# Optimization experiments

Measured on AMD Instinct MI355X. Metric: run time of the kernel, lower is better.

## Reference

```python
import jax, jax.numpy as jnp
import numpy as np
from jax import lax

B, S, H = 64, 512, 768
L = 20          # num_labels
MAX_SPANS = 8   # span_number_classifier has MAX_SPANS+1 outputs


def setup_inputs() -> dict:
    key = jax.random.key(0)
    k = jax.random.split(key, 8)
    w = lambda i, shape: jax.random.normal(k[i], shape, jnp.float32) * 0.02
    return {
        "tokens_rep": jax.random.normal(k[0], (B, S, H), jnp.float32),
        "seq_rep": jax.random.normal(k[1], (B, H), jnp.float32),
        "w_start": w(2, (H,)), "b_start": jnp.zeros((), jnp.float32),
        "w_end": w(3, (H,)), "b_end": jnp.zeros((), jnp.float32),
        "W_nspans": w(4, (H, MAX_SPANS + 1)), "b_nspans": jnp.zeros((MAX_SPANS + 1,), jnp.float32),
        "W_span": w(5, (H, L)), "b_span": jnp.zeros((L,), jnp.float32),
        "W_pol": w(6, (H + L, L)), "b_pol": jnp.zeros((L,), jnp.float32),
    }


def _select_spans(ss, es, n_spans):
    """Faithful port of get_top_spans_nongreedy's while-loop.
    ss/es: [MAX_SPANS] ascending-sorted top indices (sentinel S beyond n_spans).
    Each iteration advances s_idx and/or e_idx, so 2*MAX_SPANS steps suffice."""
    def body(i, st):
        s_idx, e_idx, last_end, rem, out_s, out_e, cnt = st
        active = (rem > 0) & (s_idx < n_spans) & (e_idx < n_spans)
        s = ss[jnp.minimum(s_idx, MAX_SPANS - 1)]
        e = es[jnp.minimum(e_idx, MAX_SPANS - 1)]
        accept = active & (e > s) & (s >= last_end)
        inc_e = active & (~accept) & (e <= s)
        inc_s = active & (~accept) & (e > s)
        out_s = jnp.where(accept, out_s.at[cnt].set(s), out_s)
        out_e = jnp.where(accept, out_e.at[cnt].set(e), out_e)
        last_end = jnp.where(accept, e, last_end)
        a = accept.astype(jnp.int32)
        return (s_idx + a + inc_s.astype(jnp.int32),
                e_idx + a + inc_e.astype(jnp.int32),
                last_end, rem - a, out_s, out_e, cnt + a)

    z = jnp.zeros((MAX_SPANS,), jnp.int32)
    init = (jnp.int32(0), jnp.int32(0), jnp.int32(0), n_spans, z, z, jnp.int32(0))
    st = lax.fori_loop(0, 2 * MAX_SPANS, body, init)
    return st[4], st[5], st[6]  # starts, ends, count


def _per_item(tokens, starts, ends, fsl, n_spans, W_span, b_span):
    # sigmoid is monotone, so top-k of sigmoid(logits) == top-k of logits
    _, i_s = lax.top_k(starts, MAX_SPANS)
    _, i_e = lax.top_k(ends, MAX_SPANS)
    rank = jnp.arange(MAX_SPANS)
    keep = rank < n_spans
    ss = jnp.sort(jnp.where(keep, i_s, S).astype(jnp.int32))  # sentinel S sorts last
    es = jnp.sort(jnp.where(keep, i_e, S).astype(jnp.int32))
    out_s, out_e, cnt = _select_spans(ss, es, n_spans)
    valid = rank < cnt
    vf = valid.astype(tokens.dtype)

    # span mean-pooling tokens[s:e+1].mean(0) via a [MAX_SPANS,S] mask matmul
    t = jnp.arange(S)
    span_mask = ((t[None, :] >= out_s[:, None]) & (t[None, :] <= out_e[:, None])).astype(tokens.dtype)
    lengths = (out_e - out_s + 1).astype(tokens.dtype)
    span_vecs = (span_mask @ tokens) / lengths[:, None]         # [MAX_SPANS, H]

    mls = jax.nn.softmax(span_vecs @ W_span + b_span, axis=1)   # [MAX_SPANS, L]
    span_labels = jnp.argmax(mls, axis=1)
    fsl_soft = jax.nn.softmax(fsl)
    has_valid = cnt > 0

    labels_oh_m = jnp.zeros((L,), tokens.dtype).at[span_labels].max(vf)
    labels_oh_m = jnp.where(has_valid, labels_oh_m,
                            jnp.zeros((L,), tokens.dtype).at[jnp.argmax(fsl_soft)].set(1.0))
    spans_m = jnp.max(jnp.where(valid[:, None], mls, -jnp.inf), axis=0)
    spans_m = jnp.where(has_valid, spans_m, jnp.zeros((L,), tokens.dtype))
    starts_oh_m = jnp.zeros((S,), tokens.dtype).at[out_s].max(vf)
    ends_oh_m = jnp.zeros((S,), tokens.dtype).at[out_e].max(vf)

    # n_spans <= 1 branch
    labels_oh_1 = jnp.zeros((L,), tokens.dtype).at[jnp.argmax(fsl_soft)].set(1.0)
    starts_oh_1 = jnp.zeros((S,), tokens.dtype).at[jnp.argmax(starts)].set(1.0)
    ends_oh_1 = jnp.zeros((S,), tokens.dtype).at[jnp.argmax(ends)].set(1.0)

    single = n_spans <= 1
    spans = jnp.where(single, fsl_soft, spans_m)
    labels_oh = jnp.where(single, labels_oh_1, labels_oh_m)
    starts_oh = jnp.where(single, starts_oh_1, starts_oh_m)
    ends_oh = jnp.where(single, ends_oh_1, ends_oh_m)
    return spans, starts_oh, ends_oh, labels_oh


def reference(tokens_rep, seq_rep, w_start, b_start, w_end, b_end,
              W_nspans, b_nspans, W_span, b_span, W_pol, b_pol):
    full_seq_logits = seq_rep @ W_span + b_span        # [B, L]
    start_logits = tokens_rep @ w_start + b_start      # [B, S]
    end_logits = tokens_rep @ w_end + b_end            # [B, S]
    n_spans_logits = seq_rep @ W_nspans + b_nspans     # [B, MAX_SPANS+1]
    all_n_spans = jnp.argmax(n_spans_logits, axis=1).astype(jnp.int32)

    spans, starts_oh, ends_oh, labels_oh = jax.vmap(
        _per_item, in_axes=(0, 0, 0, 0, 0, None, None)
    )(tokens_rep, start_logits, end_logits, full_seq_logits, all_n_spans, W_span, b_span)

    pol_logits = jnp.concatenate([seq_rep, spans], axis=1) @ W_pol + b_pol
    return (start_logits, end_logits, spans, n_spans_logits, pol_logits,
            starts_oh, ends_oh, labels_oh)
```

## Files before the change

kernel.cpp:

```cpp
#include <hip/hip_runtime.h>
#include <math.h>

#define NB 64
#define SS 512
#define HH 768
#define LL 20
#define MS 8
#define NSPC 9

#define OFF_START 0
#define OFF_END   (NB*SS)
#define OFF_SPANS (2*NB*SS)
#define OFF_NSP   (2*NB*SS + NB*LL)
#define OFF_POL   (2*NB*SS + NB*LL + NB*NSPC)
#define OFF_SOH   (2*NB*SS + 2*NB*LL + NB*NSPC)
#define OFF_EOH   (3*NB*SS + 2*NB*LL + NB*NSPC)
#define OFF_LOH   (4*NB*SS + 2*NB*LL + NB*NSPC)

struct WS {
  float fsl[NB][LL];
  float mls[NB][MS][LL];
  int   nspans[NB];
  int   fslarg[NB];
  int   cnt[NB];
  int   out_s[NB][MS];
  int   out_e[NB][MS];
  int   slabel[NB][MS];
};

__global__ __launch_bounds__(256) void k0_seq(
    const float* __restrict__ seq,
    const float* __restrict__ Wspan, const float* __restrict__ bspan,
    const float* __restrict__ Wnsp,  const float* __restrict__ bnsp,
    float* __restrict__ out, WS* __restrict__ ws)
{
  int b = blockIdx.x;
  __shared__ float sh[HH];
  __shared__ float logits[LL + NSPC];
  int t = threadIdx.x;
  for (int i = t; i < HH; i += 256) sh[i] = seq[b*HH + i];
  __syncthreads();
  int wave = t >> 6, lane = t & 63;
  for (int o = wave; o < LL + NSPC; o += 4) {
    float acc = 0.f;
    if (o < LL) {
      for (int k = 0; k < HH/64; ++k) { int h = lane + 64*k; acc += sh[h] * Wspan[h*LL + o]; }
    } else {
      int j = o - LL;
      for (int k = 0; k < HH/64; ++k) { int h = lane + 64*k; acc += sh[h] * Wnsp[h*NSPC + j]; }
    }
    for (int off = 32; off >= 1; off >>= 1) acc += __shfl_down(acc, off);
    if (lane == 0) logits[o] = acc + (o < LL ? bspan[o] : bnsp[o - LL]);
  }
  __syncthreads();
  if (t == 0) {
    int bi = 0; float bv = logits[LL];
    for (int j = 1; j < NSPC; ++j) { float v = logits[LL + j]; if (v > bv) { bv = v; bi = j; } }
    ws->nspans[b] = bi;
    int fi = 0; float fv = logits[0];
    for (int j = 1; j < LL; ++j) { float v = logits[j]; if (v > fv) { fv = v; fi = j; } }
    ws->fslarg[b] = fi;
  }
  if (t < LL)  ws->fsl[b][t] = logits[t];
  if (t < NSPC) out[OFF_NSP + b*NSPC + t] = logits[LL + t];
}

__global__ __launch_bounds__(256) void k1_logits(
    const float4* __restrict__ tok,
    const float* __restrict__ wstart, const float* __restrict__ bstart,
    const float* __restrict__ wend,  const float* __restrict__ bend,
    float* __restrict__ out)
{
  __shared__ float4 shs[HH/4], she[HH/4];
  int t = threadIdx.x;
  const float4* wsg = (const float4*)wstart;
  const float4* weg = (const float4*)wend;
  for (int i = t; i < HH/4; i += 256) { shs[i] = wsg[i]; she[i] = weg[i]; }
  __syncthreads();
  int wave = t >> 6, lane = t & 63;
  int r = blockIdx.x * 4 + wave;
  const float4* row = tok + (size_t)r * (HH/4);
  float as = 0.f, ae = 0.f;
  for (int k = 0; k < 3; ++k) {
    int idx = k*64 + lane;
    float4 x = row[idx];
    float4 a = shs[idx]; float4 c = she[idx];
    as += x.x*a.x + x.y*a.y + x.z*a.z + x.w*a.w;
    ae += x.x*c.x + x.y*c.y + x.z*c.z + x.w*c.w;
  }
  for (int off = 32; off >= 1; off >>= 1) { as += __shfl_down(as, off); ae += __shfl_down(ae, off); }
  if (lane == 0) {
    out[OFF_START + r] = as + bstart[0];
    out[OFF_END   + r] = ae + bend[0];
  }
}

__global__ __launch_bounds__(256) void k2_select(
    float* __restrict__ out, WS* __restrict__ ws)
{
  int b = blockIdx.x;
  int t = threadIdx.x;
  int wave = t >> 6, lane = t & 63;

  __shared__ float candV[2][32];
  __shared__ int   candI[2][32];
  __shared__ int   topI[2][MS];
  __shared__ int   sh_cnt, sh_single;
  __shared__ int   sh_os[MS], sh_oe[MS];

  float sv0 = out[OFF_START + b*SS + t];
  float sv1 = out[OFF_START + b*SS + t + 256];
  float ev0 = out[OFF_END   + b*SS + t];
  float ev1 = out[OFF_END   + b*SS + t + 256];
  int   si0 = t, si1 = t + 256, ei0 = t, ei1 = t + 256;

  #pragma unroll
  for (int k = 0; k < MS; ++k) {
    float lvS = sv0; int liS = si0;
    if (sv1 > lvS) { lvS = sv1; liS = si1; }
    float lvE = ev0; int liE = ei0;
    if (ev1 > lvE) { lvE = ev1; liE = ei1; }
    #pragma unroll
    for (int m = 32; m >= 1; m >>= 1) {
      float ovS = __shfl_xor(lvS, m); int oiS = __shfl_xor(liS, m);
      if (ovS > lvS || (ovS == lvS && oiS < liS)) { lvS = ovS; liS = oiS; }
      float ovE = __shfl_xor(lvE, m); int oiE = __shfl_xor(liE, m);
      if (ovE > lvE || (ovE == lvE && oiE < liE)) { lvE = ovE; liE = oiE; }
    }
    if (lane == 0) {
      candV[0][wave*MS + k] = lvS; candI[0][wave*MS + k] = liS;
      candV[1][wave*MS + k] = lvE; candI[1][wave*MS + k] = liE;
    }
    if (si0 == liS) sv0 = -INFINITY;
    if (si1 == liS) sv1 = -INFINITY;
    if (ei0 == liE) ev0 = -INFINITY;
    if (ei1 == liE) ev1 = -INFINITY;
  }
  __syncthreads();

  if (wave < 2) {
    float v = -INFINITY; int idx = 0x7fffffff;
    if (lane < 32) { v = candV[wave][lane]; idx = candI[wave][lane]; }
    int rank = 0;
    #pragma unroll
    for (int j = 0; j < 32; ++j) {
      float vj = __shfl(v, j); int ij = __shfl(idx, j);
      if (vj > v || (vj == v && ij < idx)) ++rank;
    }
    if (lane < 32 && rank < MS) topI[wave][rank] = idx;
  }
  __syncthreads();

  if (wave == 0) {
    int n = ws->nspans[b];
    int xs = SS, xe = SS;
    if (lane < MS && lane < n) { xs = topI[0][lane]; xe = topI[1][lane]; }
    int rs = 0, re = 0;
    #pragma unroll
    for (int j = 0; j < MS; ++j) {
      int xj = __shfl(xs, j);
      if (xj < xs || (xj == xs && j < lane)) ++rs;
      int yj = __shfl(xe, j);
      if (yj < xe || (yj == xe && j < lane)) ++re;
    }
    int ss_srt = 0, es_srt = 0;
    #pragma unroll
    for (int j = 0; j < MS; ++j) {
      int xj = __shfl(xs, j); int rj = __shfl(rs, j);
      if (rj == lane) ss_srt = xj;
      int yj = __shfl(xe, j); int qj = __shfl(re, j);
      if (qj == lane) es_srt = yj;
    }
    int si = 0, ei = 0, last = 0, rem = n, cnt = 0;
    int my_os = 0, my_oe = 0;
    for (int it = 0; it < 2*MS; ++it) {
      bool active = (rem > 0) && (si < n) && (ei < n);
      int s = __shfl(ss_srt, si < MS ? si : MS - 1);
      int e = __shfl(es_srt, ei < MS ? ei : MS - 1);
      bool accept = active && (e > s) && (s >= last);
      bool ince = active && !accept && (e <= s);
      bool incs = active && !accept && (e > s);
      if (accept) {
        if (lane == cnt) { my_os = s; my_oe = e; }
        last = e; ++cnt; --rem; ++si; ++ei;
      } else {
        si += incs ? 1 : 0; ei += ince ? 1 : 0;
      }
    }
    if (lane < MS) {
      sh_os[lane] = my_os; sh_oe[lane] = my_oe;
      ws->out_s[b][lane] = my_os; ws->out_e[b][lane] = my_oe;
    }
    if (lane == 0) {
      sh_cnt = cnt; sh_single = (n <= 1) ? 1 : 0;
      ws->cnt[b] = cnt;
    }
  }
  __syncthreads();

  int cnt = sh_cnt, single = sh_single;
  for (int pos = t; pos < SS; pos += 256) {
    float sval = 0.f, eval = 0.f;
    if (single) {
      if (pos == topI[0][0]) sval = 1.f;
      if (pos == topI[1][0]) eval = 1.f;
    } else {
      for (int i = 0; i < cnt; ++i) {
        if (pos == sh_os[i]) sval = 1.f;
        if (pos == sh_oe[i]) eval = 1.f;
      }
    }
    out[OFF_SOH + b*SS + pos] = sval;
    out[OFF_EOH + b*SS + pos] = eval;
  }
}

__global__ __launch_bounds__(1024) void k3_pool(
    const float4* __restrict__ tok,
    const float* __restrict__ Wspan, const float* __restrict__ bspan,
    WS* __restrict__ ws)
{
  int b = blockIdx.x >> 3;
  int i = blockIdx.x & (MS - 1);
  if (i >= ws->cnt[b]) return;
  int s0 = ws->out_s[b][i], e0 = ws->out_e[b][i];
  int t = threadIdx.x;
  int g = t >> 8;
  int tid = t & 255;

  __shared__ float4 part[4][HH/4];
  __shared__ float pooled[HH];
  __shared__ float lg[LL];

  if (tid < HH/4) {
    float4 acc = make_float4(0.f, 0.f, 0.f, 0.f);
    const float4* base = tok + (size_t)b * SS * (HH/4) + tid;
    #pragma unroll 4
    for (int r = s0 + g; r <= e0; r += 4) {
      float4 x = base[(size_t)r * (HH/4)];
      acc.x += x.x; acc.y += x.y; acc.z += x.z; acc.w += x.w;
    }
    part[g][tid] = acc;
  }
  __syncthreads();

  if (t < HH/4) {
    float4 p0 = part[0][t], p1 = part[1][t], p2 = part[2][t], p3 = part[3][t];
    float inv = 1.f / (float)(e0 - s0 + 1);
    float4 s;
    s.x = (p0.x + p1.x + p2.x + p3.x) * inv;
    s.y = (p0.y + p1.y + p2.y + p3.y) * inv;
    s.z = (p0.z + p1.z + p2.z + p3.z) * inv;
    s.w = (p0.w + p1.w + p2.w + p3.w) * inv;
    ((float4*)pooled)[t] = s;
  }
  __syncthreads();

  int wave = t >> 6, lane = t & 63;
  for (int l = wave; l < LL; l += 16) {
    float acc = 0.f;
    for (int k = 0; k < HH/64; ++k) { int h = lane + 64*k; acc += pooled[h] * Wspan[h*LL + l]; }
    for (int off = 32; off >= 1; off >>= 1) acc += __shfl_down(acc, off);
    if (lane == 0) lg[l] = acc + bspan[l];
  }
  __syncthreads();

  if (t == 0) {
    float v[LL]; float mx = -INFINITY;
    #pragma unroll
    for (int l = 0; l < LL; ++l) { v[l] = lg[l]; mx = fmaxf(mx, v[l]); }
    int am = 0; float av = v[0];
    #pragma unroll
    for (int l = 1; l < LL; ++l) if (v[l] > av) { av = v[l]; am = l; }
    float sum = 0.f;
    #pragma unroll
    for (int l = 0; l < LL; ++l) { v[l] = expf(v[l] - mx); sum += v[l]; }
    float isum = 1.f / sum;
    #pragma unroll
    for (int l = 0; l < LL; ++l) ws->mls[b][i][l] = v[l] * isum;
    ws->slabel[b][i] = am;
  }
}

__global__ __launch_bounds__(256) void k4_final(
    const float* __restrict__ seq,
    const float* __restrict__ Wpol, const float* __restrict__ bpol,
    float* __restrict__ out, WS* __restrict__ ws)
{
  int b = blockIdx.x;
  int t = threadIdx.x;
  __shared__ float sp[LL];
  __shared__ float fsl_soft[LL];
  int n = ws->nspans[b];
  int single = (n <= 1) ? 1 : 0;
  int cnt = ws->cnt[b];
  int fa = ws->fslarg[b];
  if (t == 0) {
    float lg[LL]; float mx = -INFINITY;
    #pragma unroll
    for (int l = 0; l < LL; ++l) { lg[l] = ws->fsl[b][l]; mx = fmaxf(mx, lg[l]); }
    float sum = 0.f;
    #pragma unroll
    for (int l = 0; l < LL; ++l) { lg[l] = expf(lg[l] - mx); sum += lg[l]; }
    float isum = 1.f / sum;
    #pragma unroll
    for (int l = 0; l < LL; ++l) fsl_soft[l] = lg[l] * isum;
  }
  __syncthreads();
  if (t < LL) {
    float v;
    if (single) v = fsl_soft[t];
    else if (cnt > 0) { v = -INFINITY; for (int i = 0; i < cnt; ++i) v = fmaxf(v, ws->mls[b][i][t]); }
    else v = 0.f;
    sp[t] = v;
    out[OFF_SPANS + b*LL + t] = v;
    float lo = 0.f;
    if (single || cnt == 0) lo = (t == fa) ? 1.f : 0.f;
    else { for (int i = 0; i < cnt; ++i) if (ws->slabel[b][i] == t) lo = 1.f; }
    out[OFF_LOH + b*LL + t] = lo;
  }
  __syncthreads();
  int wave = t >> 6, lane = t & 63;
  const float* seqb = seq + b*HH;
  for (int l = wave; l < LL; l += 4) {
    float acc = 0.f;
    for (int k = 0; k < 13; ++k) {
      int h = lane + 64*k;
      if (h < HH + LL) {
        float v = (h < HH) ? seqb[h] : sp[h - HH];
        acc += v * Wpol[h*LL + l];
      }
    }
    for (int off = 32; off >= 1; off >>= 1) acc += __shfl_down(acc, off);
    if (lane == 0) out[OFF_POL + b*LL + l] = acc + bpol[l];
  }
}

extern "C" void kernel_launch(void* const* d_in, const int* in_sizes, int n_in,
                              void* d_out, int out_size, void* d_ws, size_t ws_size,
                              hipStream_t stream)
{
  const float* tok    = (const float*)d_in[0];
  const float* seq    = (const float*)d_in[1];
  const float* wstart = (const float*)d_in[2];
  const float* bstart = (const float*)d_in[3];
  const float* wend   = (const float*)d_in[4];
  const float* bend   = (const float*)d_in[5];
  const float* Wnsp   = (const float*)d_in[6];
  const float* bnsp   = (const float*)d_in[7];
  const float* Wspan  = (const float*)d_in[8];
  const float* bspan  = (const float*)d_in[9];
  const float* Wpol   = (const float*)d_in[10];
  const float* bpol   = (const float*)d_in[11];
  float* out = (float*)d_out;
  WS* ws = (WS*)d_ws;

  k0_seq  <<<NB, 256, 0, stream>>>(seq, Wspan, bspan, Wnsp, bnsp, out, ws);
  k1_logits<<<NB*SS/4, 256, 0, stream>>>((const float4*)tok, wstart, bstart, wend, bend, out);
  k2_select<<<NB, 256, 0, stream>>>(out, ws);
  k3_pool <<<NB*MS, 1024, 0, stream>>>((const float4*)tok, Wspan, bspan, ws);
  k4_final<<<NB, 256, 0, stream>>>(seq, Wpol, bpol, out, ws);
}
```

Before: 87.72 us.

## Fuse five kernels into two and process four token rows per wave

Merges the seq-logit kernel with the start/end logit kernel into one launch, with the blocks split by index, and has each wave compute four token rows instead of one. It also fuses span selection, span pooling, label softmax and the polarity head into a single 1024-thread block per batch item, keeping intermediates in shared memory instead of workspace. This removes three kernel launches and the global round-trips between them. The cost is that span pooling now runs serially per span inside only 64 blocks rather than across 512 blocks, which lowers parallelism on the pooling reads.

```diff
diff --git a/kernel.cpp b/kernel.cpp
--- a/kernel.cpp
+++ b/kernel.cpp
@@ -19,83 +19,90 @@
 
 struct WS {
   float fsl[NB][LL];
-  float mls[NB][MS][LL];
   int   nspans[NB];
   int   fslarg[NB];
-  int   cnt[NB];
-  int   out_s[NB][MS];
-  int   out_e[NB][MS];
-  int   slabel[NB][MS];
 };
 
-__global__ __launch_bounds__(256) void k0_seq(
+__global__ __launch_bounds__(256) void kA(
+    const float4* __restrict__ tok,
+    const float* __restrict__ wstart, const float* __restrict__ bstart,
+    const float* __restrict__ wend,  const float* __restrict__ bend,
     const float* __restrict__ seq,
     const float* __restrict__ Wspan, const float* __restrict__ bspan,
     const float* __restrict__ Wnsp,  const float* __restrict__ bnsp,
     float* __restrict__ out, WS* __restrict__ ws)
 {
-  int b = blockIdx.x;
-  __shared__ float sh[HH];
-  __shared__ float logits[LL + NSPC];
   int t = threadIdx.x;
-  for (int i = t; i < HH; i += 256) sh[i] = seq[b*HH + i];
-  __syncthreads();
   int wave = t >> 6, lane = t & 63;
-  for (int o = wave; o < LL + NSPC; o += 4) {
-    float acc = 0.f;
-    if (o < LL) {
-      for (int k = 0; k < HH/64; ++k) { int h = lane + 64*k; acc += sh[h] * Wspan[h*LL + o]; }
-    } else {
-      int j = o - LL;
-      for (int k = 0; k < HH/64; ++k) { int h = lane + 64*k; acc += sh[h] * Wnsp[h*NSPC + j]; }
-    }
-    for (int off = 32; off >= 1; off >>= 1) acc += __shfl_down(acc, off);
-    if (lane == 0) logits[o] = acc + (o < LL ? bspan[o] : bnsp[o - LL]);
-  }
-  __syncthreads();
-  if (t == 0) {
-    int bi = 0; float bv = logits[LL];
-    for (int j = 1; j < NSPC; ++j) { float v = logits[LL + j]; if (v > bv) { bv = v; bi = j; } }
-    ws->nspans[b] = bi;
-    int fi = 0; float fv = logits[0];
-    for (int j = 1; j < LL; ++j) { float v = logits[j]; if (v > fv) { fv = v; fi = j; } }
-    ws->fslarg[b] = fi;
-  }
-  if (t < LL)  ws->fsl[b][t] = logits[t];
-  if (t < NSPC) out[OFF_NSP + b*NSPC + t] = logits[LL + t];
+
+  if (blockIdx.x < 2048) {
+    __shared__ float4 shs[HH/4], she[HH/4];
+    const float4* wsg = (const float4*)wstart;
+    const float4* weg = (const float4*)wend;
+    for (int i = t; i < HH/4; i += 256) { shs[i] = wsg[i]; she[i] = weg[i]; }
+    __syncthreads();
+    int r0 = blockIdx.x * 16 + wave * 4;
+    const float4* base = tok + (size_t)r0 * (HH/4);
+    float as[4] = {0.f,0.f,0.f,0.f}, ae[4] = {0.f,0.f,0.f,0.f};
+    #pragma unroll
+    for (int k = 0; k < 3; ++k) {
+      int idx = k*64 + lane;
+      float4 a = shs[idx], c = she[idx];
+      #pragma unroll
+      for (int j = 0; j < 4; ++j) {
+        float4 x = base[(size_t)j * (HH/4) + idx];
+        as[j] += x.x*a.x + x.y*a.y + x.z*a.z + x.w*a.w;
+        ae[j] += x.x*c.x + x.y*c.y + x.z*c.z + x.w*c.w;
+      }
+    }
+    float b0 = bstart[0], b1 = bend[0];
+    #pragma unroll
+    for (int j = 0; j < 4; ++j) {
+      float a = as[j], e = ae[j];
+      for (int off = 32; off >= 1; off >>= 1) { a += __shfl_down(a, off); e += __shfl_down(e, off); }
+      if (lane == 0) {
+        out[OFF_START + r0 + j] = a + b0;
+        out[OFF_END   + r0 + j] = e + b1;
+      }
+    }
+  } else {
+    int b = blockIdx.x - 2048;
+    __shared__ float sh[HH];
+    __shared__ float logits[LL + NSPC];
+    for (int i = t; i < HH; i += 256) sh[i] = seq[b*HH + i];
+    __syncthreads();
+    for (int o = wave; o < LL + NSPC; o += 4) {
+      float acc = 0.f;
+      if (o < LL) {
+        for (int k = 0; k < HH/64; ++k) { int h = lane + 64*k; acc += sh[h] * Wspan[h*LL + o]; }
+      } else {
+        int j = o - LL;
+        for (int k = 0; k < HH/64; ++k) { int h = lane + 64*k; acc += sh[h] * Wnsp[h*NSPC + j]; }
+      }
+      for (int off = 32; off >= 1; off >>= 1) acc += __shfl_down(acc, off);
+      if (lane == 0) logits[o] = acc + (o < LL ? bspan[o] : bnsp[o - LL]);
+    }
+    __syncthreads();
+    if (t == 0) {
+      int bi = 0; float bv = logits[LL];
+      #pragma unroll
+      for (int j = 1; j < NSPC; ++j) { float v = logits[LL + j]; if (v > bv) { bv = v; bi = j; } }
+      ws->nspans[b] = bi;
+      int fi = 0; float fv = logits[0];
+      #pragma unroll
+      for (int j = 1; j < LL; ++j) { float v = logits[j]; if (v > fv) { fv = v; fi = j; } }
+      ws->fslarg[b] = fi;
+    }
+    if (t < LL)  ws->fsl[b][t] = logits[t];
+    if (t < NSPC) out[OFF_NSP + b*NSPC + t] = logits[LL + t];
+  }
 }
 
-__global__ __launch_bounds__(256) void k1_logits(
+__global__ __launch_bounds__(1024) void kBC(
     const float4* __restrict__ tok,
-    const float* __restrict__ wstart, const float* __restrict__ bstart,
-    const float* __restrict__ wend,  const float* __restrict__ bend,
-    float* __restrict__ out)
-{
-  __shared__ float4 shs[HH/4], she[HH/4];
-  int t = threadIdx.x;
-  const float4* wsg = (const float4*)wstart;
-  const float4* weg = (const float4*)wend;
-  for (int i = t; i < HH/4; i += 256) { shs[i] = wsg[i]; she[i] = weg[i]; }
-  __syncthreads();
-  int wave = t >> 6, lane = t & 63;
-  int r = blockIdx.x * 4 + wave;
-  const float4* row = tok + (size_t)r * (HH/4);
-  float as = 0.f, ae = 0.f;
-  for (int k = 0; k < 3; ++k) {
-    int idx = k*64 + lane;
-    float4 x = row[idx];
-    float4 a = shs[idx]; float4 c = she[idx];
-    as += x.x*a.x + x.y*a.y + x.z*a.z + x.w*a.w;
-    ae += x.x*c.x + x.y*c.y + x.z*c.z + x.w*c.w;
-  }
-  for (int off = 32; off >= 1; off >>= 1) { as += __shfl_down(as, off); ae += __shfl_down(ae, off); }
-  if (lane == 0) {
-    out[OFF_START + r] = as + bstart[0];
-    out[OFF_END   + r] = ae + bend[0];
-  }
-}
-
-__global__ __launch_bounds__(256) void k2_select(
+    const float* __restrict__ Wspan, const float* __restrict__ bspan,
+    const float* __restrict__ seq,
+    const float* __restrict__ Wpol, const float* __restrict__ bpol,
     float* __restrict__ out, WS* __restrict__ ws)
 {
   int b = blockIdx.x;
@@ -107,52 +114,61 @@
   __shared__ int   topI[2][MS];
   __shared__ int   sh_cnt, sh_single;
   __shared__ int   sh_os[MS], sh_oe[MS];
-
-  float sv0 = out[OFF_START + b*SS + t];
-  float sv1 = out[OFF_START + b*SS + t + 256];
-  float ev0 = out[OFF_END   + b*SS + t];
-  float ev1 = out[OFF_END   + b*SS + t + 256];
-  int   si0 = t, si1 = t + 256, ei0 = t, ei1 = t + 256;
-
-  #pragma unroll
-  for (int k = 0; k < MS; ++k) {
-    float lvS = sv0; int liS = si0;
-    if (sv1 > lvS) { lvS = sv1; liS = si1; }
-    float lvE = ev0; int liE = ei0;
-    if (ev1 > lvE) { lvE = ev1; liE = ei1; }
-    #pragma unroll
-    for (int m = 32; m >= 1; m >>= 1) {
-      float ovS = __shfl_xor(lvS, m); int oiS = __shfl_xor(liS, m);
-      if (ovS > lvS || (ovS == lvS && oiS < liS)) { lvS = ovS; liS = oiS; }
-      float ovE = __shfl_xor(lvE, m); int oiE = __shfl_xor(liE, m);
-      if (ovE > lvE || (ovE == lvE && oiE < liE)) { lvE = ovE; liE = oiE; }
-    }
-    if (lane == 0) {
-      candV[0][wave*MS + k] = lvS; candI[0][wave*MS + k] = liS;
-      candV[1][wave*MS + k] = lvE; candI[1][wave*MS + k] = liE;
-    }
-    if (si0 == liS) sv0 = -INFINITY;
-    if (si1 == liS) sv1 = -INFINITY;
-    if (ei0 == liE) ev0 = -INFINITY;
-    if (ei1 == liE) ev1 = -INFINITY;
-  }
-  __syncthreads();
-
-  if (wave < 2) {
+  __shared__ float4 part[5][HH/4];
+  __shared__ float pooled[HH];
+  __shared__ float slg[LL];
+  __shared__ float mls_s[MS][LL];
+  __shared__ int   slab_s[MS];
+  __shared__ float sp[LL], fsl_soft[LL];
+
+  int n = ws->nspans[b];
+
+  if (t < 256) {
+    float sv0 = out[OFF_START + b*SS + t];
+    float sv1 = out[OFF_START + b*SS + t + 256];
+    float ev0 = out[OFF_END   + b*SS + t];
+    float ev1 = out[OFF_END   + b*SS + t + 256];
+    int   si0 = t, si1 = t + 256, ei0 = t, ei1 = t + 256;
+    #pragma unroll
+    for (int k = 0; k < MS; ++k) {
+      float lvS = sv0; int liS = si0;
+      if (sv1 > lvS) { lvS = sv1; liS = si1; }
+      float lvE = ev0; int liE = ei0;
+      if (ev1 > lvE) { lvE = ev1; liE = ei1; }
+      #pragma unroll
+      for (int m = 32; m >= 1; m >>= 1) {
+        float ovS = __shfl_xor(lvS, m); int oiS = __shfl_xor(liS, m);
+        if (ovS > lvS || (ovS == lvS && oiS < liS)) { lvS = ovS; liS = oiS; }
+        float ovE = __shfl_xor(lvE, m); int oiE = __shfl_xor(liE, m);
+        if (ovE > lvE || (ovE == lvE && oiE < liE)) { lvE = ovE; liE = oiE; }
+      }
+      if (lane == 0) {
+        candV[0][wave*MS + k] = lvS; candI[0][wave*MS + k] = liS;
+        candV[1][wave*MS + k] = lvE; candI[1][wave*MS + k] = liE;
+      }
+      if (si0 == liS) sv0 = -INFINITY;
+      if (si1 == liS) sv1 = -INFINITY;
+      if (ei0 == liE) ev0 = -INFINITY;
+      if (ei1 == liE) ev1 = -INFINITY;
+    }
+  }
+  __syncthreads();
+
+  if (t < 128) {
+    int w = wave;
     float v = -INFINITY; int idx = 0x7fffffff;
-    if (lane < 32) { v = candV[wave][lane]; idx = candI[wave][lane]; }
+    if (lane < 32) { v = candV[w][lane]; idx = candI[w][lane]; }
     int rank = 0;
     #pragma unroll
     for (int j = 0; j < 32; ++j) {
       float vj = __shfl(v, j); int ij = __shfl(idx, j);
       if (vj > v || (vj == v && ij < idx)) ++rank;
     }
-    if (lane < 32 && rank < MS) topI[wave][rank] = idx;
+    if (lane < 32 && rank < MS) topI[w][rank] = idx;
   }
   __syncthreads();
 
   if (wave == 0) {
-    int n = ws->nspans[b];
     int xs = SS, xe = SS;
     if (lane < MS && lane < n) { xs = topI[0][lane]; xe = topI[1][lane]; }
     int rs = 0, re = 0;
@@ -187,19 +203,15 @@
         si += incs ? 1 : 0; ei += ince ? 1 : 0;
       }
     }
-    if (lane < MS) {
-      sh_os[lane] = my_os; sh_oe[lane] = my_oe;
-      ws->out_s[b][lane] = my_os; ws->out_e[b][lane] = my_oe;
-    }
-    if (lane == 0) {
-      sh_cnt = cnt; sh_single = (n <= 1) ? 1 : 0;
-      ws->cnt[b] = cnt;
-    }
+    if (lane < MS) { sh_os[lane] = my_os; sh_oe[lane] = my_oe; }
+    if (lane == 0) { sh_cnt = cnt; sh_single = (n <= 1) ? 1 : 0; }
   }
   __syncthreads();
 
   int cnt = sh_cnt, single = sh_single;
-  for (int pos = t; pos < SS; pos += 256) {
+
+  if (t < SS) {
+    int pos = t;
     float sval = 0.f, eval = 0.f;
     if (single) {
       if (pos == topI[0][0]) sval = 1.f;
@@ -213,87 +225,57 @@
     out[OFF_SOH + b*SS + pos] = sval;
     out[OFF_EOH + b*SS + pos] = eval;
   }
-}
-
-__global__ __launch_bounds__(1024) void k3_pool(
-    const float4* __restrict__ tok,
-    const float* __restrict__ Wspan, const float* __restrict__ bspan,
-    WS* __restrict__ ws)
-{
-  int b = blockIdx.x >> 3;
-  int i = blockIdx.x & (MS - 1);
-  if (i >= ws->cnt[b]) return;
-  int s0 = ws->out_s[b][i], e0 = ws->out_e[b][i];
-  int t = threadIdx.x;
-  int g = t >> 8;
-  int tid = t & 255;
-
-  __shared__ float4 part[4][HH/4];
-  __shared__ float pooled[HH];
-  __shared__ float lg[LL];
-
-  if (tid < HH/4) {
-    float4 acc = make_float4(0.f, 0.f, 0.f, 0.f);
-    const float4* base = tok + (size_t)b * SS * (HH/4) + tid;
-    #pragma unroll 4
-    for (int r = s0 + g; r <= e0; r += 4) {
-      float4 x = base[(size_t)r * (HH/4)];
-      acc.x += x.x; acc.y += x.y; acc.z += x.z; acc.w += x.w;
-    }
-    part[g][tid] = acc;
-  }
-  __syncthreads();
-
-  if (t < HH/4) {
-    float4 p0 = part[0][t], p1 = part[1][t], p2 = part[2][t], p3 = part[3][t];
-    float inv = 1.f / (float)(e0 - s0 + 1);
-    float4 s;
-    s.x = (p0.x + p1.x + p2.x + p3.x) * inv;
-    s.y = (p0.y + p1.y + p2.y + p3.y) * inv;
-    s.z = (p0.z + p1.z + p2.z + p3.z) * inv;
-    s.w = (p0.w + p1.w + p2.w + p3.w) * inv;
-    ((float4*)pooled)[t] = s;
-  }
-  __syncthreads();
-
-  int wave = t >> 6, lane = t & 63;
-  for (int l = wave; l < LL; l += 16) {
-    float acc = 0.f;
-    for (int k = 0; k < HH/64; ++k) { int h = lane + 64*k; acc += pooled[h] * Wspan[h*LL + l]; }
-    for (int off = 32; off >= 1; off >>= 1) acc += __shfl_down(acc, off);
-    if (lane == 0) lg[l] = acc + bspan[l];
-  }
-  __syncthreads();
-
-  if (t == 0) {
-    float v[LL]; float mx = -INFINITY;
-    #pragma unroll
-    for (int l = 0; l < LL; ++l) { v[l] = lg[l]; mx = fmaxf(mx, v[l]); }
-    int am = 0; float av = v[0];
-    #pragma unroll
-    for (int l = 1; l < LL; ++l) if (v[l] > av) { av = v[l]; am = l; }
-    float sum = 0.f;
-    #pragma unroll
-    for (int l = 0; l < LL; ++l) { v[l] = expf(v[l] - mx); sum += v[l]; }
-    float isum = 1.f / sum;
-    #pragma unroll
-    for (int l = 0; l < LL; ++l) ws->mls[b][i][l] = v[l] * isum;
-    ws->slabel[b][i] = am;
-  }
-}
-
-__global__ __launch_bounds__(256) void k4_final(
-    const float* __restrict__ seq,
-    const float* __restrict__ Wpol, const float* __restrict__ bpol,
-    float* __restrict__ out, WS* __restrict__ ws)
-{
-  int b = blockIdx.x;
-  int t = threadIdx.x;
-  __shared__ float sp[LL];
-  __shared__ float fsl_soft[LL];
-  int n = ws->nspans[b];
-  int single = (n <= 1) ? 1 : 0;
-  int cnt = ws->cnt[b];
+
+  int g = t / 192, q = t - g * 192;
+  for (int i = 0; i < cnt; ++i) {
+    int s0 = sh_os[i], e0 = sh_oe[i];
+    if (t < 960) {
+      float4 acc = make_float4(0.f, 0.f, 0.f, 0.f);
+      const float4* base = tok + (size_t)b * SS * (HH/4) + q;
+      #pragma unroll 4
+      for (int r = s0 + g; r <= e0; r += 5) {
+        float4 x = base[(size_t)r * (HH/4)];
+        acc.x += x.x; acc.y += x.y; acc.z += x.z; acc.w += x.w;
+      }
+      part[g][q] = acc;
+    }
+    __syncthreads();
+    if (t < HH/4) {
+      float inv = 1.f / (float)(e0 - s0 + 1);
+      float4 p0 = part[0][t], p1 = part[1][t], p2 = part[2][t], p3 = part[3][t], p4 = part[4][t];
+      float4 s;
+      s.x = (p0.x + p1.x + p2.x + p3.x + p4.x) * inv;
+      s.y = (p0.y + p1.y + p2.y + p3.y + p4.y) * inv;
+      s.z = (p0.z + p1.z + p2.z + p3.z + p4.z) * inv;
+      s.w = (p0.w + p1.w + p2.w + p3.w + p4.w) * inv;
+      ((float4*)pooled)[t] = s;
+    }
+    __syncthreads();
+    for (int l = wave; l < LL; l += 16) {
+      float acc = 0.f;
+      for (int k = 0; k < HH/64; ++k) { int h = lane + 64*k; acc += pooled[h] * Wspan[h*LL + l]; }
+      for (int off = 32; off >= 1; off >>= 1) acc += __shfl_down(acc, off);
+      if (lane == 0) slg[l] = acc + bspan[l];
+    }
+    __syncthreads();
+    if (t == 0) {
+      float v[LL]; float mx = -INFINITY;
+      #pragma unroll
+      for (int l = 0; l < LL; ++l) { v[l] = slg[l]; mx = fmaxf(mx, v[l]); }
+      int am = 0; float av = v[0];
+      #pragma unroll
+      for (int l = 1; l < LL; ++l) if (v[l] > av) { av = v[l]; am = l; }
+      float sum = 0.f;
+      #pragma unroll
+      for (int l = 0; l < LL; ++l) { v[l] = expf(v[l] - mx); sum += v[l]; }
+      float isum = 1.f / sum;
+      #pragma unroll
+      for (int l = 0; l < LL; ++l) mls_s[i][l] = v[l] * isum;
+      slab_s[i] = am;
+    }
+    __syncthreads();
+  }
+
   int fa = ws->fslarg[b];
   if (t == 0) {
     float lg[LL]; float mx = -INFINITY;
@@ -310,19 +292,18 @@
   if (t < LL) {
     float v;
     if (single) v = fsl_soft[t];
-    else if (cnt > 0) { v = -INFINITY; for (int i = 0; i < cnt; ++i) v = fmaxf(v, ws->mls[b][i][t]); }
+    else if (cnt > 0) { v = -INFINITY; for (int i = 0; i < cnt; ++i) v = fmaxf(v, mls_s[i][t]); }
     else v = 0.f;
     sp[t] = v;
     out[OFF_SPANS + b*LL + t] = v;
     float lo = 0.f;
     if (single || cnt == 0) lo = (t == fa) ? 1.f : 0.f;
-    else { for (int i = 0; i < cnt; ++i) if (ws->slabel[b][i] == t) lo = 1.f; }
+    else { for (int i = 0; i < cnt; ++i) if (slab_s[i] == t) lo = 1.f; }
     out[OFF_LOH + b*LL + t] = lo;
   }
   __syncthreads();
-  int wave = t >> 6, lane = t & 63;
   const float* seqb = seq + b*HH;
-  for (int l = wave; l < LL; l += 4) {
+  for (int l = wave; l < LL; l += 16) {
     float acc = 0.f;
     for (int k = 0; k < 13; ++k) {
       int h = lane + 64*k;
@@ -355,9 +336,8 @@
   float* out = (float*)d_out;
   WS* ws = (WS*)d_ws;
 
-  k0_seq  <<<NB, 256, 0, stream>>>(seq, Wspan, bspan, Wnsp, bnsp, out, ws);
-  k1_logits<<<NB*SS/4, 256, 0, stream>>>((const float4*)tok, wstart, bstart, wend, bend, out);
-  k2_select<<<NB, 256, 0, stream>>>(out, ws);
-  k3_pool <<<NB*MS, 1024, 0, stream>>>((const float4*)tok, Wspan, bspan, ws);
-  k4_final<<<NB, 256, 0, stream>>>(seq, Wpol, bpol, out, ws);
+  kA <<<2112, 256, 0, stream>>>((const float4*)tok, wstart, bstart, wend, bend,
+                                seq, Wspan, bspan, Wnsp, bnsp, out, ws);
+  kBC<<<NB, 1024, 0, stream>>>((const float4*)tok, Wspan, bspan,
+                               seq, Wpol, bpol, out, ws);
 }
```

Result: slower. 90.32 us (+3.0%).

## Merge seq-logit and token-logit kernels, process eight rows per wave

Applied to the files above, without the earlier changes.

Fuses the sequence-level classifier kernel and the start/end token-logit kernel into one launch. The first 1024 blocks compute start/end logits and the last 64 compute the sequence logits. Each wave now handles eight token rows instead of one, so the weight reads from shared memory are reused across rows, there are fewer blocks, and more loads are in flight. This removes one kernel launch and the weight-staging overhead per row. In exchange it uses more registers and runs fewer, longer blocks on the memory-bound pass over tokens.

```diff
diff --git a/kernel.cpp b/kernel.cpp
--- a/kernel.cpp
+++ b/kernel.cpp
@@ -28,74 +28,83 @@
   int   slabel[NB][MS];
 };
 
-__global__ __launch_bounds__(256) void k0_seq(
+__global__ __launch_bounds__(256) void kA(
+    const float4* __restrict__ tok,
+    const float* __restrict__ wstart, const float* __restrict__ bstart,
+    const float* __restrict__ wend,  const float* __restrict__ bend,
     const float* __restrict__ seq,
     const float* __restrict__ Wspan, const float* __restrict__ bspan,
     const float* __restrict__ Wnsp,  const float* __restrict__ bnsp,
     float* __restrict__ out, WS* __restrict__ ws)
 {
-  int b = blockIdx.x;
-  __shared__ float sh[HH];
-  __shared__ float logits[LL + NSPC];
   int t = threadIdx.x;
-  for (int i = t; i < HH; i += 256) sh[i] = seq[b*HH + i];
-  __syncthreads();
   int wave = t >> 6, lane = t & 63;
-  for (int o = wave; o < LL + NSPC; o += 4) {
-    float acc = 0.f;
-    if (o < LL) {
-      for (int k = 0; k < HH/64; ++k) { int h = lane + 64*k; acc += sh[h] * Wspan[h*LL + o]; }
-    } else {
-      int j = o - LL;
-      for (int k = 0; k < HH/64; ++k) { int h = lane + 64*k; acc += sh[h] * Wnsp[h*NSPC + j]; }
-    }
-    for (int off = 32; off >= 1; off >>= 1) acc += __shfl_down(acc, off);
-    if (lane == 0) logits[o] = acc + (o < LL ? bspan[o] : bnsp[o - LL]);
-  }
-  __syncthreads();
-  if (t == 0) {
-    int bi = 0; float bv = logits[LL];
-    for (int j = 1; j < NSPC; ++j) { float v = logits[LL + j]; if (v > bv) { bv = v; bi = j; } }
-    ws->nspans[b] = bi;
-    int fi = 0; float fv = logits[0];
-    for (int j = 1; j < LL; ++j) { float v = logits[j]; if (v > fv) { fv = v; fi = j; } }
-    ws->fslarg[b] = fi;
-  }
-  if (t < LL)  ws->fsl[b][t] = logits[t];
-  if (t < NSPC) out[OFF_NSP + b*NSPC + t] = logits[LL + t];
-}
-
-__global__ __launch_bounds__(256) void k1_logits(
-    const float4* __restrict__ tok,
-    const float* __restrict__ wstart, const float* __restrict__ bstart,
-    const float* __restrict__ wend,  const float* __restrict__ bend,
-    float* __restrict__ out)
-{
-  __shared__ float4 shs[HH/4], she[HH/4];
-  int t = threadIdx.x;
-  const float4* wsg = (const float4*)wstart;
-  const float4* weg = (const float4*)wend;
-  for (int i = t; i < HH/4; i += 256) { shs[i] = wsg[i]; she[i] = weg[i]; }
-  __syncthreads();
-  int wave = t >> 6, lane = t & 63;
-  int r = blockIdx.x * 4 + wave;
-  const float4* row = tok + (size_t)r * (HH/4);
-  float as = 0.f, ae = 0.f;
-  for (int k = 0; k < 3; ++k) {
-    int idx = k*64 + lane;
-    float4 x = row[idx];
-    float4 a = shs[idx]; float4 c = she[idx];
-    as += x.x*a.x + x.y*a.y + x.z*a.z + x.w*a.w;
-    ae += x.x*c.x + x.y*c.y + x.z*c.z + x.w*c.w;
-  }
-  for (int off = 32; off >= 1; off >>= 1) { as += __shfl_down(as, off); ae += __shfl_down(ae, off); }
-  if (lane == 0) {
-    out[OFF_START + r] = as + bstart[0];
-    out[OFF_END   + r] = ae + bend[0];
-  }
-}
-
-__global__ __launch_bounds__(256) void k2_select(
+
+  if (blockIdx.x < 1024) {
+    __shared__ float4 shs[HH/4], she[HH/4];
+    const float4* wsg = (const float4*)wstart;
+    const float4* weg = (const float4*)wend;
+    for (int i = t; i < HH/4; i += 256) { shs[i] = wsg[i]; she[i] = weg[i]; }
+    __syncthreads();
+    int r0 = blockIdx.x * 32 + wave * 8;
+    const float4* base = tok + (size_t)r0 * (HH/4);
+    float as[8] = {0.f,0.f,0.f,0.f,0.f,0.f,0.f,0.f};
+    float ae[8] = {0.f,0.f,0.f,0.f,0.f,0.f,0.f,0.f};
+    #pragma unroll
+    for (int k = 0; k < 3; ++k) {
+      int idx = k*64 + lane;
+      float4 a = shs[idx], c = she[idx];
+      #pragma unroll
+      for (int j = 0; j < 8; ++j) {
+        float4 x = base[(size_t)j * (HH/4) + idx];
+        as[j] += x.x*a.x + x.y*a.y + x.z*a.z + x.w*a.w;
+        ae[j] += x.x*c.x + x.y*c.y + x.z*c.z + x.w*c.w;
+      }
+    }
+    float b0 = bstart[0], b1 = bend[0];
+    #pragma unroll
+    for (int j = 0; j < 8; ++j) {
+      float a = as[j], e = ae[j];
+      for (int off = 32; off >= 1; off >>= 1) { a += __shfl_down(a, off); e += __shfl_down(e, off); }
+      if (lane == 0) {
+        out[OFF_START + r0 + j] = a + b0;
+        out[OFF_END   + r0 + j] = e + b1;
+      }
+    }
+  } else {
+    int b = blockIdx.x - 1024;
+    __shared__ float sh[HH];
+    __shared__ float logits[LL + NSPC];
+    for (int i = t; i < HH; i += 256) sh[i] = seq[b*HH + i];
+    __syncthreads();
+    for (int o = wave; o < LL + NSPC; o += 4) {
+      float acc = 0.f;
+      if (o < LL) {
+        for (int k = 0; k < HH/64; ++k) { int h = lane + 64*k; acc += sh[h] * Wspan[h*LL + o]; }
+      } else {
+        int j = o - LL;
+        for (int k = 0; k < HH/64; ++k) { int h = lane + 64*k; acc += sh[h] * Wnsp[h*NSPC + j]; }
+      }
+      for (int off = 32; off >= 1; off >>= 1) acc += __shfl_down(acc, off);
+      if (lane == 0) logits[o] = acc + (o < LL ? bspan[o] : bnsp[o - LL]);
+    }
+    __syncthreads();
+    if (t == 0) {
+      int bi = 0; float bv = logits[LL];
+      #pragma unroll
+      for (int j = 1; j < NSPC; ++j) { float v = logits[LL + j]; if (v > bv) { bv = v; bi = j; } }
+      ws->nspans[b] = bi;
+      int fi = 0; float fv = logits[0];
+      #pragma unroll
+      for (int j = 1; j < LL; ++j) { float v = logits[j]; if (v > fv) { fv = v; fi = j; } }
+      ws->fslarg[b] = fi;
+    }
+    if (t < LL)  ws->fsl[b][t] = logits[t];
+    if (t < NSPC) out[OFF_NSP + b*NSPC + t] = logits[LL + t];
+  }
+}
+
+__global__ __launch_bounds__(256) void kB(
     float* __restrict__ out, WS* __restrict__ ws)
 {
   int b = blockIdx.x;
@@ -215,7 +224,7 @@
   }
 }
 
-__global__ __launch_bounds__(1024) void k3_pool(
+__global__ __launch_bounds__(1024) void kC(
     const float4* __restrict__ tok,
     const float* __restrict__ Wspan, const float* __restrict__ bspan,
     WS* __restrict__ ws)
@@ -282,7 +291,7 @@
   }
 }
 
-__global__ __launch_bounds__(256) void k4_final(
+__global__ __launch_bounds__(256) void kD(
     const float* __restrict__ seq,
     const float* __restrict__ Wpol, const float* __restrict__ bpol,
     float* __restrict__ out, WS* __restrict__ ws)
@@ -355,9 +364,9 @@
   float* out = (float*)d_out;
   WS* ws = (WS*)d_ws;
 
-  k0_seq  <<<NB, 256, 0, stream>>>(seq, Wspan, bspan, Wnsp, bnsp, out, ws);
-  k1_logits<<<NB*SS/4, 256, 0, stream>>>((const float4*)tok, wstart, bstart, wend, bend, out);
-  k2_select<<<NB, 256, 0, stream>>>(out, ws);
-  k3_pool <<<NB*MS, 1024, 0, stream>>>((const float4*)tok, Wspan, bspan, ws);
-  k4_final<<<NB, 256, 0, stream>>>(seq, Wpol, bpol, out, ws);
-}
+  kA<<<1088, 256, 0, stream>>>((const float4*)tok, wstart, bstart, wend, bend,
+                               seq, Wspan, bspan, Wnsp, bnsp, out, ws);
+  kB<<<NB, 256, 0, stream>>>(out, ws);
+  kC<<<NB*MS, 1024, 0, stream>>>((const float4*)tok, Wspan, bspan, ws);
+  kD<<<NB, 256, 0, stream>>>(seq, Wpol, bpol, out, ws);
+}
```

Result: faster. 84.99 us (-3.1%).
